# Kernel tuning notes

Measured on AMD Instinct MI355X. Metric: run time of the kernel, lower is better.

Reference implementation:

```python
import jax, jax.numpy as jnp
import numpy as np

O_FEAT = 4096
I_FEAT = 4096
NNZ = int(0.05 * O_FEAT * I_FEAT)  # 838860, matches k = int(residual.numel()*ortho_ratio)


def setup_inputs() -> dict:
    key = jax.random.key(0)
    k_x, k_pk, k_sc, k_v, k_r, k_c = jax.random.split(key, 6)
    x = jax.random.normal(k_x, (2, 1024, I_FEAT), dtype=jnp.float32)
    # packed int4 weights: each byte holds two 4-bit codes (offset-by-8 signed int4)
    base_packed = jax.random.randint(k_pk, (O_FEAT, I_FEAT // 2), 0, 256).astype(jnp.uint8)
    # per-output-row scales (robust_max / 7), strictly positive
    scales = jax.random.uniform(k_sc, (O_FEAT,), minval=1e-4, maxval=2e-2, dtype=jnp.float32)
    # sparse residual correction in fp16 (CSR values; represented as COO triplets)
    ortho_vals = (jax.random.normal(k_v, (NNZ,), dtype=jnp.float32) * 1e-2).astype(jnp.float16)
    ortho_rows = jax.random.randint(k_r, (NNZ,), 0, O_FEAT, dtype=jnp.int32)
    ortho_cols = jax.random.randint(k_c, (NNZ,), 0, I_FEAT, dtype=jnp.int32)
    return {
        "x": x,
        "base_packed": base_packed,
        "scales": scales,
        "ortho_vals": ortho_vals,
        "ortho_rows": ortho_rows,
        "ortho_cols": ortho_cols,
        "alpha": 1.0,
    }


def _dequant_int4(base_packed, scales):
    # unpack: low nibble -> even columns, high nibble -> odd columns
    O, Ih = base_packed.shape
    low = (base_packed & jnp.uint8(0x0F)).astype(jnp.int32)
    high = (base_packed >> 4).astype(jnp.int32)
    q = jnp.stack([low, high], axis=-1).reshape(O, Ih * 2)  # interleaved [l0,h0,l1,h1,...]
    return (q - 8).astype(jnp.float32) * scales[:, None]


def reference(x, base_packed, scales, ortho_vals, ortho_rows, ortho_cols, alpha):
    O, I = base_packed.shape[0], base_packed.shape[1] * 2
    w_base = _dequant_int4(base_packed, scales)  # [O, I] f32
    # scatter sparse residual into dense weight (same math as CSR spmm residual)
    w_sparse = jnp.zeros((O, I), jnp.float32).at[ortho_rows, ortho_cols].add(
        ortho_vals.astype(jnp.float32))
    W = w_base + alpha * w_sparse
    out = jnp.einsum("bsi,oi->bso", x.astype(jnp.float32), W)
    return out.astype(x.dtype)
```

## Files before the change

### kernel.cpp

```cpp
#include <hip/hip_runtime.h>
#include <hip/hip_fp16.h>
#include <stdint.h>

#define O_FEAT 4096
#define I_FEAT 4096
#define M_DIM  2048
#define K_DIM  4096

typedef __attribute__((ext_vector_type(8))) short short8;
typedef __attribute__((ext_vector_type(2))) short short2v;
typedef __attribute__((ext_vector_type(4))) float floatx4;

#define AS1 __attribute__((address_space(1)))
#define AS3 __attribute__((address_space(3)))

__device__ __forceinline__ uint16_t f32_to_bf16(float f) {
    uint32_t u = __builtin_bit_cast(uint32_t, f);
    u = (u + 0x7FFFu + ((u >> 16) & 1u)) >> 16;
    return (uint16_t)u;
}
__device__ __forceinline__ float bf16_to_f32(uint16_t h) {
    uint32_t u = ((uint32_t)h) << 16;
    return __builtin_bit_cast(float, u);
}

__device__ __forceinline__ void load_lds16(const uint16_t* gptr, uint16_t* ldsptr) {
    __builtin_amdgcn_global_load_lds((const AS1 uint32_t*)gptr,
                                     (AS3 uint32_t*)ldsptr, 16, 0, 0);
}

__global__ __launch_bounds__(256) void dequant_kernel(
        const void*  __restrict__ packed,
        const float* __restrict__ scales,
        uint16_t*    __restrict__ W) {
    const int lane = threadIdx.x & 63;
    uint32_t probe = ((const uint32_t*)packed)[lane];
    const bool int32mode = (__ballot(probe >= 256u) == 0ull);

    int idx = blockIdx.x * 256 + threadIdx.x;
    float s = scales[idx >> 9];

    uint32_t bytes4;
    if (int32mode) {
        uint4 w = ((const uint4*)packed)[idx];
        bytes4 = (w.x & 0xFFu) | ((w.y & 0xFFu) << 8) |
                 ((w.z & 0xFFu) << 16) | ((w.w & 0xFFu) << 24);
    } else {
        bytes4 = ((const uint32_t*)packed)[idx];
    }

    uint16_t o[8];
#pragma unroll
    for (int b = 0; b < 4; ++b) {
        int byte = (bytes4 >> (8 * b)) & 0xFF;
        o[2 * b]     = f32_to_bf16((float)((byte & 0xF) - 8) * s);
        o[2 * b + 1] = f32_to_bf16((float)((byte >> 4) - 8) * s);
    }
    uint4 v;
    v.x = (uint32_t)o[0] | ((uint32_t)o[1] << 16);
    v.y = (uint32_t)o[2] | ((uint32_t)o[3] << 16);
    v.z = (uint32_t)o[4] | ((uint32_t)o[5] << 16);
    v.w = (uint32_t)o[6] | ((uint32_t)o[7] << 16);
    ((uint4*)W)[idx] = v;
}

#define SCATTER_BLOCKS 3328
__global__ __launch_bounds__(256) void scatter_xconv_kernel(
        const void*  __restrict__ vals,
        const int*   __restrict__ rows,
        const int*   __restrict__ cols,
        const float* __restrict__ alpha,
        const float* __restrict__ x,
        uint16_t*    __restrict__ W,
        uint16_t*    __restrict__ Xb,
        int nnz) {
    if (blockIdx.x < SCATTER_BLOCKS) {
        const int lane = threadIdx.x & 63;
        float p = fabsf(((const float*)vals)[lane]);
        int cnt = __popcll(__ballot(p > 1e-4f && p < 1.0f));
        const bool f32mode = (cnt >= 32);

        int i = blockIdx.x * 256 + threadIdx.x;
        if (i >= nnz) return;
        float v = f32mode ? ((const float*)vals)[i]
                          : __half2float(((const __half*)vals)[i]);
        v *= alpha[0];
        int r = rows[i], c = cols[i];
        size_t elem = (size_t)r * I_FEAT + c;

#if __has_builtin(__builtin_amdgcn_global_atomic_fadd_v2bf16)
        const bool hi = (elem & 1);
        short b = (short)f32_to_bf16(v);
        short2v val;
        val[0] = hi ? (short)0 : b;
        val[1] = hi ? b : (short)0;
        __builtin_amdgcn_global_atomic_fadd_v2bf16(
            (AS1 short2v*)(W + (elem & ~(size_t)1)), val);
#else
        uint32_t* word = (uint32_t*)W + (elem >> 1);
        bool hi = (c & 1);
        uint32_t old = *word, assumed;
        do {
            assumed = old;
            uint16_t cur = hi ? (uint16_t)(assumed >> 16) : (uint16_t)(assumed & 0xFFFF);
            uint16_t nw  = f32_to_bf16(bf16_to_f32(cur) + v);
            uint32_t neww = hi ? ((assumed & 0x0000FFFFu) | ((uint32_t)nw << 16))
                               : ((assumed & 0xFFFF0000u) | (uint32_t)nw);
            old = atomicCAS(word, assumed, neww);
        } while (old != assumed);
#endif
    } else {
        int idx = (blockIdx.x - SCATTER_BLOCKS) * 256 + threadIdx.x;
        float4 v0 = ((const float4*)x)[2 * idx];
        float4 v1 = ((const float4*)x)[2 * idx + 1];
        uint4 o;
        o.x = (uint32_t)f32_to_bf16(v0.x) | ((uint32_t)f32_to_bf16(v0.y) << 16);
        o.y = (uint32_t)f32_to_bf16(v0.z) | ((uint32_t)f32_to_bf16(v0.w) << 16);
        o.z = (uint32_t)f32_to_bf16(v1.x) | ((uint32_t)f32_to_bf16(v1.y) << 16);
        o.w = (uint32_t)f32_to_bf16(v1.z) | ((uint32_t)f32_to_bf16(v1.w) << 16);
        ((uint4*)Xb)[idx] = o;
    }
}

#define BM 128
#define BN 256
#define BK 64
#define NT (K_DIM / BK)
#define A_ELEMS (BM * BK)
#define B_ELEMS (BN * BK)
#define TILE_ELEMS (A_ELEMS + B_ELEMS)

#define MFMA16(d, a, b) d = __builtin_amdgcn_mfma_f32_16x16x32_bf16(a, b, d, 0, 0, 0)

__global__ __launch_bounds__(512, 2) void gemm_bt_kernel(
        const uint16_t* __restrict__ A,
        const uint16_t* __restrict__ B,
        float* __restrict__ C) {
    __shared__ uint16_t lds[3 * TILE_ELEMS];

    const int tid  = threadIdx.x;
    const int wave = tid >> 6;
    const int lane = tid & 63;
    const int wm   = wave >> 2;
    const int wn   = wave & 3;

    const int wgid = blockIdx.y * 16 + blockIdx.x;
    const int swz  = (wgid & 7) * 32 + (wgid >> 3);
    const int bm0  = (swz >> 4) * BM;
    const int bn0  = (swz & 15) * BN;

    const int srow = (wave << 3) + (lane >> 3);
    const int xcol = ((lane & 7) ^ (lane >> 3)) << 3;
    const uint16_t* gA0 = A + (size_t)(bm0 + srow) * K_DIM + xcol;
    const uint16_t* gA1 = gA0 + (size_t)64 * K_DIM;
    const uint16_t* gB0 = B + (size_t)(bn0 + srow) * K_DIM + xcol;
    const uint16_t* gB1 = gB0 + (size_t)64  * K_DIM;
    const uint16_t* gB2 = gB0 + (size_t)128 * K_DIM;
    const uint16_t* gB3 = gB0 + (size_t)192 * K_DIM;
    const int ldsA0 = wave * 512;
    const int ldsA1 = 4096 + wave * 512;
    const int ldsB0 = A_ELEMS + wave * 512;
    const int ldsB1 = A_ELEMS + 4096 + wave * 512;
    const int ldsB2 = A_ELEMS + 8192 + wave * 512;
    const int ldsB3 = A_ELEMS + 12288 + wave * 512;

    const int fr  = lane & 15;
    const int ko  = (lane >> 4) << 3;
    const int sk0 = (ko)      ^ ((fr & 7) << 3);
    const int sk1 = (32 + ko) ^ ((fr & 7) << 3);
    const int raA = (wm * 64 + fr) * BK;
    const int raB = A_ELEMS + (wn * 64 + fr) * BK;

    floatx4 acc[4][4];
#pragma unroll
    for (int i = 0; i < 4; ++i)
#pragma unroll
        for (int j = 0; j < 4; ++j) acc[i][j] = {0.f, 0.f, 0.f, 0.f};

    load_lds16(gA0, &lds[ldsA0]);
    load_lds16(gA1, &lds[ldsA1]);
    load_lds16(gB0, &lds[ldsB0]);
    load_lds16(gB1, &lds[ldsB1]);
    load_lds16(gB2, &lds[ldsB2]);
    load_lds16(gB3, &lds[ldsB3]);
    load_lds16(gA0 + BK, &lds[TILE_ELEMS + ldsA0]);
    load_lds16(gA1 + BK, &lds[TILE_ELEMS + ldsA1]);
    load_lds16(gB0 + BK, &lds[TILE_ELEMS + ldsB0]);
    load_lds16(gB1 + BK, &lds[TILE_ELEMS + ldsB1]);
    load_lds16(gB2 + BK, &lds[TILE_ELEMS + ldsB2]);
    load_lds16(gB3 + BK, &lds[TILE_ELEMS + ldsB3]);
    asm volatile("s_waitcnt vmcnt(6)" ::: "memory");
    __builtin_amdgcn_s_barrier();

    int cbo = 0;
    int sbo = 2 * TILE_ELEMS;

    for (int t = 0; t < NT; ++t) {
        const bool pf   = (t + 2 < NT);
        const int  kofs = (t + 2) * BK;

        short8 a00 = *(const short8*)&lds[cbo + raA + sk0];
        short8 a01 = *(const short8*)&lds[cbo + raA + sk1];
        short8 a10 = *(const short8*)&lds[cbo + raA + 1024 + sk0];
        short8 a11 = *(const short8*)&lds[cbo + raA + 1024 + sk1];
        short8 b00 = *(const short8*)&lds[cbo + raB + sk0];
        short8 b01 = *(const short8*)&lds[cbo + raB + sk1];
        short8 b10 = *(const short8*)&lds[cbo + raB + 1024 + sk0];
        short8 b11 = *(const short8*)&lds[cbo + raB + 1024 + sk1];
        if (pf) {
            load_lds16(gA0 + kofs, &lds[sbo + ldsA0]);
            load_lds16(gA1 + kofs, &lds[sbo + ldsA1]);
        }
        __builtin_amdgcn_s_barrier();
        asm volatile("s_waitcnt lgkmcnt(0)");
        __builtin_amdgcn_s_setprio(1);
        MFMA16(acc[0][0], a00, b00); MFMA16(acc[0][0], a01, b01);
        MFMA16(acc[0][1], a00, b10); MFMA16(acc[0][1], a01, b11);
        MFMA16(acc[1][0], a10, b00); MFMA16(acc[1][0], a11, b01);
        MFMA16(acc[1][1], a10, b10); MFMA16(acc[1][1], a11, b11);
        __builtin_amdgcn_s_setprio(0);
        __builtin_amdgcn_s_barrier();

        short8 b20 = *(const short8*)&lds[cbo + raB + 2048 + sk0];
        short8 b21 = *(const short8*)&lds[cbo + raB + 2048 + sk1];
        short8 b30 = *(const short8*)&lds[cbo + raB + 3072 + sk0];
        short8 b31 = *(const short8*)&lds[cbo + raB + 3072 + sk1];
        if (pf) {
            load_lds16(gB0 + kofs, &lds[sbo + ldsB0]);
            load_lds16(gB1 + kofs, &lds[sbo + ldsB1]);
        }
        __builtin_amdgcn_s_barrier();
        asm volatile("s_waitcnt lgkmcnt(0)");
        __builtin_amdgcn_s_setprio(1);
        MFMA16(acc[0][2], a00, b20); MFMA16(acc[0][2], a01, b21);
        MFMA16(acc[0][3], a00, b30); MFMA16(acc[0][3], a01, b31);
        MFMA16(acc[1][2], a10, b20); MFMA16(acc[1][2], a11, b21);
        MFMA16(acc[1][3], a10, b30); MFMA16(acc[1][3], a11, b31);
        __builtin_amdgcn_s_setprio(0);
        __builtin_amdgcn_s_barrier();

        short8 a20 = *(const short8*)&lds[cbo + raA + 2048 + sk0];
        short8 a21 = *(const short8*)&lds[cbo + raA + 2048 + sk1];
        short8 a30 = *(const short8*)&lds[cbo + raA + 3072 + sk0];
        short8 a31 = *(const short8*)&lds[cbo + raA + 3072 + sk1];
        if (pf) {
            load_lds16(gB2 + kofs, &lds[sbo + ldsB2]);
            load_lds16(gB3 + kofs, &lds[sbo + ldsB3]);
        }
        __builtin_amdgcn_s_barrier();
        asm volatile("s_waitcnt lgkmcnt(0)");
        __builtin_amdgcn_s_setprio(1);
        MFMA16(acc[2][2], a20, b20); MFMA16(acc[2][2], a21, b21);
        MFMA16(acc[2][3], a20, b30); MFMA16(acc[2][3], a21, b31);
        MFMA16(acc[3][2], a30, b20); MFMA16(acc[3][2], a31, b21);
        MFMA16(acc[3][3], a30, b30); MFMA16(acc[3][3], a31, b31);
        __builtin_amdgcn_s_setprio(0);
        __builtin_amdgcn_s_barrier();

        __builtin_amdgcn_s_setprio(1);
        MFMA16(acc[2][0], a20, b00); MFMA16(acc[2][0], a21, b01);
        MFMA16(acc[2][1], a20, b10); MFMA16(acc[2][1], a21, b11);
        MFMA16(acc[3][0], a30, b00); MFMA16(acc[3][0], a31, b01);
        MFMA16(acc[3][1], a30, b10); MFMA16(acc[3][1], a31, b11);
        __builtin_amdgcn_s_setprio(0);
        if (t + 2 < NT) {
            asm volatile("s_waitcnt vmcnt(6)" ::: "memory");
        } else if (t + 1 < NT) {
            asm volatile("s_waitcnt vmcnt(0)" ::: "memory");
        }
        if (t + 1 < NT) __builtin_amdgcn_s_barrier();

        cbo += TILE_ELEMS; if (cbo == 3 * TILE_ELEMS) cbo = 0;
        sbo += TILE_ELEMS; if (sbo == 3 * TILE_ELEMS) sbo = 0;
    }

    const int cn  = lane & 15;
    const int rb4 = (lane >> 4) * 4;
#pragma unroll
    for (int i = 0; i < 4; ++i)
#pragma unroll
        for (int j = 0; j < 4; ++j)
#pragma unroll
            for (int r = 0; r < 4; ++r) {
                const int row = bm0 + wm * 64 + i * 16 + rb4 + r;
                const int col = bn0 + wn * 64 + j * 16 + cn;
                C[(size_t)row * O_FEAT + col] = acc[i][j][r];
            }
}

extern "C" void kernel_launch(void* const* d_in, const int* in_sizes, int n_in,
                              void* d_out, int out_size, void* d_ws, size_t ws_size,
                              hipStream_t stream) {
    const float* x      = (const float*)d_in[0];
    const void*  packed = d_in[1];
    const float* scales = (const float*)d_in[2];
    const void*  vals   = d_in[3];
    const int*   rows   = (const int*)d_in[4];
    const int*   cols   = (const int*)d_in[5];
    const float* alpha  = (const float*)d_in[6];
    float*       out    = (float*)d_out;
    const int nnz = in_sizes[3];

    uint16_t* W  = (uint16_t*)d_ws;
    uint16_t* Xb = (uint16_t*)((char*)d_ws + (size_t)O_FEAT * I_FEAT * 2);

    dequant_kernel<<<8192, 256, 0, stream>>>(packed, scales, W);
    scatter_xconv_kernel<<<SCATTER_BLOCKS + 4096, 256, 0, stream>>>(
        vals, rows, cols, alpha, x, W, Xb, nnz);
    gemm_bt_kernel<<<dim3(O_FEAT / BN, M_DIM / BM), 512, 0, stream>>>(Xb, W, out);
}
```

Measured before the change: 230.3 us.

## Fuse dequant, scatter, conversion and GEMM into one cooperative persistent kernel

Replaces three kernel launches with a single cooperative launch of 256 workgroups. Grid-wide syncs separate three phases: dequantizing the weights and converting x to bf16, scattering the sparse residual with atomics, then the GEMM. The aim is to remove launch gaps and inter-kernel overhead. In exchange, the preprocessing phases now run on only 256 workgroups with grid-stride loops, which may cost memory-bandwidth parallelism, and the two grid syncs add their own cost.

```diff
diff --git a/kernel.cpp b/kernel.cpp
--- a/kernel.cpp
+++ b/kernel.cpp
@@ -1,6 +1,9 @@
 #include <hip/hip_runtime.h>
 #include <hip/hip_fp16.h>
+#include <hip/hip_cooperative_groups.h>
 #include <stdint.h>
+
+namespace cg = cooperative_groups;
 
 #define O_FEAT 4096
 #define I_FEAT 4096
@@ -27,99 +30,6 @@
 __device__ __forceinline__ void load_lds16(const uint16_t* gptr, uint16_t* ldsptr) {
     __builtin_amdgcn_global_load_lds((const AS1 uint32_t*)gptr,
                                      (AS3 uint32_t*)ldsptr, 16, 0, 0);
-}
-
-__global__ __launch_bounds__(256) void dequant_kernel(
-        const void*  __restrict__ packed,
-        const float* __restrict__ scales,
-        uint16_t*    __restrict__ W) {
-    const int lane = threadIdx.x & 63;
-    uint32_t probe = ((const uint32_t*)packed)[lane];
-    const bool int32mode = (__ballot(probe >= 256u) == 0ull);
-
-    int idx = blockIdx.x * 256 + threadIdx.x;
-    float s = scales[idx >> 9];
-
-    uint32_t bytes4;
-    if (int32mode) {
-        uint4 w = ((const uint4*)packed)[idx];
-        bytes4 = (w.x & 0xFFu) | ((w.y & 0xFFu) << 8) |
-                 ((w.z & 0xFFu) << 16) | ((w.w & 0xFFu) << 24);
-    } else {
-        bytes4 = ((const uint32_t*)packed)[idx];
-    }
-
-    uint16_t o[8];
-#pragma unroll
-    for (int b = 0; b < 4; ++b) {
-        int byte = (bytes4 >> (8 * b)) & 0xFF;
-        o[2 * b]     = f32_to_bf16((float)((byte & 0xF) - 8) * s);
-        o[2 * b + 1] = f32_to_bf16((float)((byte >> 4) - 8) * s);
-    }
-    uint4 v;
-    v.x = (uint32_t)o[0] | ((uint32_t)o[1] << 16);
-    v.y = (uint32_t)o[2] | ((uint32_t)o[3] << 16);
-    v.z = (uint32_t)o[4] | ((uint32_t)o[5] << 16);
-    v.w = (uint32_t)o[6] | ((uint32_t)o[7] << 16);
-    ((uint4*)W)[idx] = v;
-}
-
-#define SCATTER_BLOCKS 3328
-__global__ __launch_bounds__(256) void scatter_xconv_kernel(
-        const void*  __restrict__ vals,
-        const int*   __restrict__ rows,
-        const int*   __restrict__ cols,
-        const float* __restrict__ alpha,
-        const float* __restrict__ x,
-        uint16_t*    __restrict__ W,
-        uint16_t*    __restrict__ Xb,
-        int nnz) {
-    if (blockIdx.x < SCATTER_BLOCKS) {
-        const int lane = threadIdx.x & 63;
-        float p = fabsf(((const float*)vals)[lane]);
-        int cnt = __popcll(__ballot(p > 1e-4f && p < 1.0f));
-        const bool f32mode = (cnt >= 32);
-
-        int i = blockIdx.x * 256 + threadIdx.x;
-        if (i >= nnz) return;
-        float v = f32mode ? ((const float*)vals)[i]
-                          : __half2float(((const __half*)vals)[i]);
-        v *= alpha[0];
-        int r = rows[i], c = cols[i];
-        size_t elem = (size_t)r * I_FEAT + c;
-
-#if __has_builtin(__builtin_amdgcn_global_atomic_fadd_v2bf16)
-        const bool hi = (elem & 1);
-        short b = (short)f32_to_bf16(v);
-        short2v val;
-        val[0] = hi ? (short)0 : b;
-        val[1] = hi ? b : (short)0;
-        __builtin_amdgcn_global_atomic_fadd_v2bf16(
-            (AS1 short2v*)(W + (elem & ~(size_t)1)), val);
-#else
-        uint32_t* word = (uint32_t*)W + (elem >> 1);
-        bool hi = (c & 1);
-        uint32_t old = *word, assumed;
-        do {
-            assumed = old;
-            uint16_t cur = hi ? (uint16_t)(assumed >> 16) : (uint16_t)(assumed & 0xFFFF);
-            uint16_t nw  = f32_to_bf16(bf16_to_f32(cur) + v);
-            uint32_t neww = hi ? ((assumed & 0x0000FFFFu) | ((uint32_t)nw << 16))
-                               : ((assumed & 0xFFFF0000u) | (uint32_t)nw);
-            old = atomicCAS(word, assumed, neww);
-        } while (old != assumed);
-#endif
-    } else {
-        int idx = (blockIdx.x - SCATTER_BLOCKS) * 256 + threadIdx.x;
-        float4 v0 = ((const float4*)x)[2 * idx];
-        float4 v1 = ((const float4*)x)[2 * idx + 1];
-        uint4 o;
-        o.x = (uint32_t)f32_to_bf16(v0.x) | ((uint32_t)f32_to_bf16(v0.y) << 16);
-        o.y = (uint32_t)f32_to_bf16(v0.z) | ((uint32_t)f32_to_bf16(v0.w) << 16);
-        o.z = (uint32_t)f32_to_bf16(v1.x) | ((uint32_t)f32_to_bf16(v1.y) << 16);
-        o.w = (uint32_t)f32_to_bf16(v1.z) | ((uint32_t)f32_to_bf16(v1.w) << 16);
-        ((uint4*)Xb)[idx] = o;
-    }
 }
 
 #define BM 128
@@ -130,21 +40,124 @@
 #define B_ELEMS (BN * BK)
 #define TILE_ELEMS (A_ELEMS + B_ELEMS)
 
+#define NTHREADS 131072
+
 #define MFMA16(d, a, b) d = __builtin_amdgcn_mfma_f32_16x16x32_bf16(a, b, d, 0, 0, 0)
 
-__global__ __launch_bounds__(512, 2) void gemm_bt_kernel(
-        const uint16_t* __restrict__ A,
-        const uint16_t* __restrict__ B,
-        float* __restrict__ C) {
+__global__ __launch_bounds__(512, 2) void fused_kernel(
+        const void*  __restrict__ packed,
+        const float* __restrict__ scales,
+        const float* __restrict__ x,
+        const void*  __restrict__ vals,
+        const int*   __restrict__ rows,
+        const int*   __restrict__ cols,
+        const float* __restrict__ alpha,
+        uint16_t*    __restrict__ W,
+        uint16_t*    __restrict__ Xb,
+        float*       __restrict__ C,
+        int nnz) {
     __shared__ uint16_t lds[3 * TILE_ELEMS];
 
+    cg::grid_group grid = cg::this_grid();
     const int tid  = threadIdx.x;
+    const int lane = tid & 63;
+    const int gid  = blockIdx.x * 512 + tid;
+
+    {
+        uint32_t probe = ((const uint32_t*)packed)[lane];
+        const bool int32mode = (__ballot(probe >= 256u) == 0ull);
+#pragma unroll
+        for (int it = 0; it < 16; ++it) {
+            const int idx = it * NTHREADS + gid;
+            const float s = scales[idx >> 9];
+            uint32_t bytes4;
+            if (int32mode) {
+                uint4 w = ((const uint4*)packed)[idx];
+                bytes4 = (w.x & 0xFFu) | ((w.y & 0xFFu) << 8) |
+                         ((w.z & 0xFFu) << 16) | ((w.w & 0xFFu) << 24);
+            } else {
+                bytes4 = ((const uint32_t*)packed)[idx];
+            }
+            uint16_t o[8];
+#pragma unroll
+            for (int b = 0; b < 4; ++b) {
+                int byte = (bytes4 >> (8 * b)) & 0xFF;
+                o[2 * b]     = f32_to_bf16((float)((byte & 0xF) - 8) * s);
+                o[2 * b + 1] = f32_to_bf16((float)((byte >> 4) - 8) * s);
+            }
+            uint4 v;
+            v.x = (uint32_t)o[0] | ((uint32_t)o[1] << 16);
+            v.y = (uint32_t)o[2] | ((uint32_t)o[3] << 16);
+            v.z = (uint32_t)o[4] | ((uint32_t)o[5] << 16);
+            v.w = (uint32_t)o[6] | ((uint32_t)o[7] << 16);
+            ((uint4*)W)[idx] = v;
+        }
+#pragma unroll
+        for (int it = 0; it < 8; ++it) {
+            const int idx = it * NTHREADS + gid;
+            float4 v0 = ((const float4*)x)[2 * idx];
+            float4 v1 = ((const float4*)x)[2 * idx + 1];
+            uint4 o;
+            o.x = (uint32_t)f32_to_bf16(v0.x) | ((uint32_t)f32_to_bf16(v0.y) << 16);
+            o.y = (uint32_t)f32_to_bf16(v0.z) | ((uint32_t)f32_to_bf16(v0.w) << 16);
+            o.z = (uint32_t)f32_to_bf16(v1.x) | ((uint32_t)f32_to_bf16(v1.y) << 16);
+            o.w = (uint32_t)f32_to_bf16(v1.z) | ((uint32_t)f32_to_bf16(v1.w) << 16);
+            ((uint4*)Xb)[idx] = o;
+        }
+    }
+    __threadfence();
+    grid.sync();
+
+    {
+        float p = fabsf(((const float*)vals)[lane]);
+        int cnt = __popcll(__ballot(p > 1e-4f && p < 1.0f));
+        const bool f32mode = (cnt >= 32);
+        const float al = alpha[0];
+#pragma unroll
+        for (int it = 0; it < 7; ++it) {
+            const int i = it * NTHREADS + gid;
+            if (i < nnz) {
+                float v = f32mode ? ((const float*)vals)[i]
+                                  : __half2float(((const __half*)vals)[i]);
+                v *= al;
+                int r = rows[i], c = cols[i];
+                size_t elem = (size_t)r * I_FEAT + c;
+#if __has_builtin(__builtin_amdgcn_global_atomic_fadd_v2bf16)
+                const bool hi = (elem & 1);
+                short b = (short)f32_to_bf16(v);
+                short2v val;
+                val[0] = hi ? (short)0 : b;
+                val[1] = hi ? b : (short)0;
+                __builtin_amdgcn_global_atomic_fadd_v2bf16(
+                    (AS1 short2v*)(W + (elem & ~(size_t)1)), val);
+#else
+                uint32_t* word = (uint32_t*)W + (elem >> 1);
+                bool hi = (c & 1);
+                uint32_t old = *word, assumed;
+                do {
+                    assumed = old;
+                    uint16_t cur = hi ? (uint16_t)(assumed >> 16)
+                                      : (uint16_t)(assumed & 0xFFFF);
+                    uint16_t nw  = f32_to_bf16(bf16_to_f32(cur) + v);
+                    uint32_t neww = hi ? ((assumed & 0x0000FFFFu) | ((uint32_t)nw << 16))
+                                       : ((assumed & 0xFFFF0000u) | (uint32_t)nw);
+                    old = atomicCAS(word, assumed, neww);
+                } while (old != assumed);
+#endif
+            }
+        }
+    }
+    __threadfence();
+    grid.sync();
+
+    const uint16_t* __restrict__ A = Xb;
+    const uint16_t* __restrict__ B = W;
+
     const int wave = tid >> 6;
-    const int lane = tid & 63;
     const int wm   = wave >> 2;
     const int wn   = wave & 3;
 
-    const int wgid = blockIdx.y * 16 + blockIdx.x;
+    const int wgid = blockIdx.x;
     const int swz  = (wgid & 7) * 32 + (wgid >> 3);
     const int bm0  = (swz >> 4) * BM;
     const int bn0  = (swz & 15) * BN;
@@ -291,21 +304,24 @@
 extern "C" void kernel_launch(void* const* d_in, const int* in_sizes, int n_in,
                               void* d_out, int out_size, void* d_ws, size_t ws_size,
                               hipStream_t stream) {
-    const float* x      = (const float*)d_in[0];
     const void*  packed = d_in[1];
     const float* scales = (const float*)d_in[2];
+    const float* x      = (const float*)d_in[0];
     const void*  vals   = d_in[3];
     const int*   rows   = (const int*)d_in[4];
     const int*   cols   = (const int*)d_in[5];
     const float* alpha  = (const float*)d_in[6];
     float*       out    = (float*)d_out;
-    const int nnz = in_sizes[3];
+    int          nnz    = in_sizes[3];
 
     uint16_t* W  = (uint16_t*)d_ws;
     uint16_t* Xb = (uint16_t*)((char*)d_ws + (size_t)O_FEAT * I_FEAT * 2);
 
-    dequant_kernel<<<8192, 256, 0, stream>>>(packed, scales, W);
-    scatter_xconv_kernel<<<SCATTER_BLOCKS + 4096, 256, 0, stream>>>(
-        vals, rows, cols, alpha, x, W, Xb, nnz);
-    gemm_bt_kernel<<<dim3(O_FEAT / BN, M_DIM / BM), 512, 0, stream>>>(Xb, W, out);
-}
+    void* args[] = {
+        (void*)&packed, (void*)&scales, (void*)&x, (void*)&vals,
+        (void*)&rows, (void*)&cols, (void*)&alpha,
+        (void*)&W, (void*)&Xb, (void*)&out, (void*)&nnz
+    };
+    hipLaunchCooperativeKernel((const void*)fused_kernel, dim3(256), dim3(512),
+                               args, 0, stream);
+}
```

Measured after the change: 429.1 us. +86.3%, slower.

## Shrink GEMM tile to 128x128 with 4 waves and double-buffered LDS

Applied to the files above, without the earlier changes.

The bf16 GEMM moves from a 128x256 tile with 8 waves and triple-buffered LDS to a 128x128 tile with 4 waves and double buffering. The grid becomes 32x16 with an adjusted swizzle. The goal is more workgroups and higher occupancy with less LDS per block, so the 256 CUs stay better balanced. In exchange there is less operand reuse per tile, more total global/L2 traffic, and a shallower prefetch with a full vmcnt(0) wait every iteration.

```diff
diff --git a/kernel.cpp b/kernel.cpp
--- a/kernel.cpp
+++ b/kernel.cpp
@@ -123,53 +123,43 @@
 }
 
 #define BM 128
-#define BN 256
+#define BN 128
 #define BK 64
 #define NT (K_DIM / BK)
-#define A_ELEMS (BM * BK)
-#define B_ELEMS (BN * BK)
-#define TILE_ELEMS (A_ELEMS + B_ELEMS)
+#define BUF_ELEMS 16384
 
 #define MFMA16(d, a, b) d = __builtin_amdgcn_mfma_f32_16x16x32_bf16(a, b, d, 0, 0, 0)
 
-__global__ __launch_bounds__(512, 2) void gemm_bt_kernel(
+__global__ __launch_bounds__(256, 2) void gemm_bt_kernel(
         const uint16_t* __restrict__ A,
         const uint16_t* __restrict__ B,
         float* __restrict__ C) {
-    __shared__ uint16_t lds[3 * TILE_ELEMS];
+    __shared__ uint16_t lds[2 * BUF_ELEMS];
 
     const int tid  = threadIdx.x;
     const int wave = tid >> 6;
     const int lane = tid & 63;
-    const int wm   = wave >> 2;
-    const int wn   = wave & 3;
-
-    const int wgid = blockIdx.y * 16 + blockIdx.x;
-    const int swz  = (wgid & 7) * 32 + (wgid >> 3);
-    const int bm0  = (swz >> 4) * BM;
-    const int bn0  = (swz & 15) * BN;
-
-    const int srow = (wave << 3) + (lane >> 3);
-    const int xcol = ((lane & 7) ^ (lane >> 3)) << 3;
-    const uint16_t* gA0 = A + (size_t)(bm0 + srow) * K_DIM + xcol;
-    const uint16_t* gA1 = gA0 + (size_t)64 * K_DIM;
-    const uint16_t* gB0 = B + (size_t)(bn0 + srow) * K_DIM + xcol;
-    const uint16_t* gB1 = gB0 + (size_t)64  * K_DIM;
-    const uint16_t* gB2 = gB0 + (size_t)128 * K_DIM;
-    const uint16_t* gB3 = gB0 + (size_t)192 * K_DIM;
-    const int ldsA0 = wave * 512;
-    const int ldsA1 = 4096 + wave * 512;
-    const int ldsB0 = A_ELEMS + wave * 512;
-    const int ldsB1 = A_ELEMS + 4096 + wave * 512;
-    const int ldsB2 = A_ELEMS + 8192 + wave * 512;
-    const int ldsB3 = A_ELEMS + 12288 + wave * 512;
+    const int wm   = wave >> 1;
+    const int wn   = wave & 1;
+
+    const int wgid = blockIdx.y * 32 + blockIdx.x;
+    const int swz  = (wgid & 7) * 64 + (wgid >> 3);
+    const int bm0  = (swz >> 5) * BM;
+    const int bn0  = (swz & 31) * BN;
+
+    const int sr   = lane >> 3;
+    const int xcol = ((lane & 7) ^ sr) << 3;
+    const uint16_t* gA = A + (size_t)(bm0 + wave * 32 + sr) * K_DIM + xcol;
+    const uint16_t* gB = B + (size_t)(bn0 + wave * 32 + sr) * K_DIM + xcol;
+    const int ldsA = (wave * 32) * 64;
+    const int ldsB = 8192 + (wave * 32) * 64;
 
     const int fr  = lane & 15;
     const int ko  = (lane >> 4) << 3;
     const int sk0 = (ko)      ^ ((fr & 7) << 3);
     const int sk1 = (32 + ko) ^ ((fr & 7) << 3);
     const int raA = (wm * 64 + fr) * BK;
-    const int raB = A_ELEMS + (wn * 64 + fr) * BK;
+    const int raB = 8192 + (wn * 64 + fr) * BK;
 
     floatx4 acc[4][4];
 #pragma unroll
@@ -177,39 +167,33 @@
 #pragma unroll
         for (int j = 0; j < 4; ++j) acc[i][j] = {0.f, 0.f, 0.f, 0.f};
 
-    load_lds16(gA0, &lds[ldsA0]);
-    load_lds16(gA1, &lds[ldsA1]);
-    load_lds16(gB0, &lds[ldsB0]);
-    load_lds16(gB1, &lds[ldsB1]);
-    load_lds16(gB2, &lds[ldsB2]);
-    load_lds16(gB3, &lds[ldsB3]);
-    load_lds16(gA0 + BK, &lds[TILE_ELEMS + ldsA0]);
-    load_lds16(gA1 + BK, &lds[TILE_ELEMS + ldsA1]);
-    load_lds16(gB0 + BK, &lds[TILE_ELEMS + ldsB0]);
-    load_lds16(gB1 + BK, &lds[TILE_ELEMS + ldsB1]);
-    load_lds16(gB2 + BK, &lds[TILE_ELEMS + ldsB2]);
-    load_lds16(gB3 + BK, &lds[TILE_ELEMS + ldsB3]);
-    asm volatile("s_waitcnt vmcnt(6)" ::: "memory");
+#pragma unroll
+    for (int c = 0; c < 4; ++c)
+        load_lds16(gA + (size_t)(c * 8) * K_DIM, &lds[ldsA + c * 512]);
+#pragma unroll
+    for (int c = 0; c < 4; ++c)
+        load_lds16(gB + (size_t)(c * 8) * K_DIM, &lds[ldsB + c * 512]);
+    asm volatile("s_waitcnt vmcnt(0)" ::: "memory");
     __builtin_amdgcn_s_barrier();
 
-    int cbo = 0;
-    int sbo = 2 * TILE_ELEMS;
-
     for (int t = 0; t < NT; ++t) {
-        const bool pf   = (t + 2 < NT);
-        const int  kofs = (t + 2) * BK;
-
-        short8 a00 = *(const short8*)&lds[cbo + raA + sk0];
-        short8 a01 = *(const short8*)&lds[cbo + raA + sk1];
-        short8 a10 = *(const short8*)&lds[cbo + raA + 1024 + sk0];
-        short8 a11 = *(const short8*)&lds[cbo + raA + 1024 + sk1];
-        short8 b00 = *(const short8*)&lds[cbo + raB + sk0];
-        short8 b01 = *(const short8*)&lds[cbo + raB + sk1];
-        short8 b10 = *(const short8*)&lds[cbo + raB + 1024 + sk0];
-        short8 b11 = *(const short8*)&lds[cbo + raB + 1024 + sk1];
-        if (pf) {
-            load_lds16(gA0 + kofs, &lds[sbo + ldsA0]);
-            load_lds16(gA1 + kofs, &lds[sbo + ldsA1]);
+        const int cb = (t & 1) * BUF_ELEMS;
+        const int sb = cb ^ BUF_ELEMS;
+        const bool pf = (t + 1 < NT);
+        const size_t kofs = (size_t)(t + 1) * BK;
+
+        short8 a00 = *(const short8*)&lds[cb + raA + sk0];
+        short8 a01 = *(const short8*)&lds[cb + raA + sk1];
+        short8 a10 = *(const short8*)&lds[cb + raA + 1024 + sk0];
+        short8 a11 = *(const short8*)&lds[cb + raA + 1024 + sk1];
+        short8 b00 = *(const short8*)&lds[cb + raB + sk0];
+        short8 b01 = *(const short8*)&lds[cb + raB + sk1];
+        short8 b10 = *(const short8*)&lds[cb + raB + 1024 + sk0];
+        short8 b11 = *(const short8*)&lds[cb + raB + 1024 + sk1];
+        if (pf) {
+            load_lds16(gA + kofs,                     &lds[sb + ldsA]);
+            load_lds16(gA + kofs + (size_t)8 * K_DIM, &lds[sb + ldsA + 512]);
+            load_lds16(gA + kofs + (size_t)16 * K_DIM,&lds[sb + ldsA + 1024]);
         }
         __builtin_amdgcn_s_barrier();
         asm volatile("s_waitcnt lgkmcnt(0)");
@@ -221,13 +205,14 @@
         __builtin_amdgcn_s_setprio(0);
         __builtin_amdgcn_s_barrier();
 
-        short8 b20 = *(const short8*)&lds[cbo + raB + 2048 + sk0];
-        short8 b21 = *(const short8*)&lds[cbo + raB + 2048 + sk1];
-        short8 b30 = *(const short8*)&lds[cbo + raB + 3072 + sk0];
-        short8 b31 = *(const short8*)&lds[cbo + raB + 3072 + sk1];
-        if (pf) {
-            load_lds16(gB0 + kofs, &lds[sbo + ldsB0]);
-            load_lds16(gB1 + kofs, &lds[sbo + ldsB1]);
+        short8 b20 = *(const short8*)&lds[cb + raB + 2048 + sk0];
+        short8 b21 = *(const short8*)&lds[cb + raB + 2048 + sk1];
+        short8 b30 = *(const short8*)&lds[cb + raB + 3072 + sk0];
+        short8 b31 = *(const short8*)&lds[cb + raB + 3072 + sk1];
+        if (pf) {
+            load_lds16(gA + kofs + (size_t)24 * K_DIM,&lds[sb + ldsA + 1536]);
+            load_lds16(gB + kofs,                     &lds[sb + ldsB]);
+            load_lds16(gB + kofs + (size_t)8 * K_DIM, &lds[sb + ldsB + 512]);
         }
         __builtin_amdgcn_s_barrier();
         asm volatile("s_waitcnt lgkmcnt(0)");
@@ -239,13 +224,13 @@
         __builtin_amdgcn_s_setprio(0);
         __builtin_amdgcn_s_barrier();
 
-        short8 a20 = *(const short8*)&lds[cbo + raA + 2048 + sk0];
-        short8 a21 = *(const short8*)&lds[cbo + raA + 2048 + sk1];
-        short8 a30 = *(const short8*)&lds[cbo + raA + 3072 + sk0];
-        short8 a31 = *(const short8*)&lds[cbo + raA + 3072 + sk1];
-        if (pf) {
-            load_lds16(gB2 + kofs, &lds[sbo + ldsB2]);
-            load_lds16(gB3 + kofs, &lds[sbo + ldsB3]);
+        short8 a20 = *(const short8*)&lds[cb + raA + 2048 + sk0];
+        short8 a21 = *(const short8*)&lds[cb + raA + 2048 + sk1];
+        short8 a30 = *(const short8*)&lds[cb + raA + 3072 + sk0];
+        short8 a31 = *(const short8*)&lds[cb + raA + 3072 + sk1];
+        if (pf) {
+            load_lds16(gB + kofs + (size_t)16 * K_DIM,&lds[sb + ldsB + 1024]);
+            load_lds16(gB + kofs + (size_t)24 * K_DIM,&lds[sb + ldsB + 1536]);
         }
         __builtin_amdgcn_s_barrier();
         asm volatile("s_waitcnt lgkmcnt(0)");
@@ -263,15 +248,10 @@
         MFMA16(acc[3][0], a30, b00); MFMA16(acc[3][0], a31, b01);
         MFMA16(acc[3][1], a30, b10); MFMA16(acc[3][1], a31, b11);
         __builtin_amdgcn_s_setprio(0);
-        if (t + 2 < NT) {
-            asm volatile("s_waitcnt vmcnt(6)" ::: "memory");
-        } else if (t + 1 < NT) {
+        if (pf) {
             asm volatile("s_waitcnt vmcnt(0)" ::: "memory");
-        }
-        if (t + 1 < NT) __builtin_amdgcn_s_barrier();
-
-        cbo += TILE_ELEMS; if (cbo == 3 * TILE_ELEMS) cbo = 0;
-        sbo += TILE_ELEMS; if (sbo == 3 * TILE_ELEMS) sbo = 0;
+            __builtin_amdgcn_s_barrier();
+        }
     }
 
     const int cn  = lane & 15;
@@ -307,5 +287,5 @@
     dequant_kernel<<<8192, 256, 0, stream>>>(packed, scales, W);
     scatter_xconv_kernel<<<SCATTER_BLOCKS + 4096, 256, 0, stream>>>(
         vals, rows, cols, alpha, x, W, Xb, nnz);
-    gemm_bt_kernel<<<dim3(O_FEAT / BN, M_DIM / BM), 512, 0, stream>>>(Xb, W, out);
-}
+    gemm_bt_kernel<<<dim3(32, 16), 256, 0, stream>>>(Xb, W, out);
+}
```

New measurement: 227.0 us (median of 2 runs). Within noise of the previous version (-1.4%).
